# Optimization experiments

Measured on AMD Instinct MI355X. Metric: run time of the kernel, lower is better.

## Reference

```python
import jax, jax.numpy as jnp
import numpy as np

LOG2 = float(np.log(2.0))

def ssp(x):
    # shifted softplus used by SchNet
    return jax.nn.softplus(x) - LOG2

def setup_inputs() -> dict:
    N, E, DIM, RBF = 100000, 1600000, 64, 64
    key = jax.random.key(0)
    ks = jax.random.split(key, 20)
    def w(k, fan_in, fan_out):
        # xavier_uniform
        lim = float(np.sqrt(6.0 / (fan_in + fan_out)))
        return jax.random.uniform(k, (fan_in, fan_out), jnp.float32, -lim, lim)
    inp = {
        "node_feats": jax.random.normal(ks[0], (N, DIM), jnp.float32),
        "edge_feats": jax.random.normal(ks[1], (E, RBF), jnp.float32),
        "src": jax.random.randint(ks[2], (E,), 0, N, jnp.int32),
        "dst": jax.random.randint(ks[3], (E,), 0, N, jnp.int32),
        # EdgeUpdate.project_edge: Linear(2*dim+rbf, 2*dim) -> ssp -> Linear(2*dim, rbf)
        "eu_w1": w(ks[4], 2 * DIM + RBF, 2 * DIM), "eu_b1": jnp.zeros((2 * DIM,), jnp.float32),
        "eu_w2": w(ks[5], 2 * DIM, RBF), "eu_b2": jnp.zeros((RBF,), jnp.float32),
        # EUCFConv.project_node1: Linear(dim, dim) -> ssp (output unused by the original forward)
        "pn1_w": w(ks[6], DIM, DIM), "pn1_b": jnp.zeros((DIM,), jnp.float32),
        # EUCFConv.project_edge: Linear(rbf, dim) -> ssp -> Linear(dim, dim)
        "pe_w1": w(ks[7], RBF, DIM), "pe_b1": jnp.zeros((DIM,), jnp.float32),
        "pe_w2": w(ks[8], DIM, DIM), "pe_b2": jnp.zeros((DIM,), jnp.float32),
        # EUCFConv.project_node2: Linear(dim, dim) -> ssp -> Linear(dim, dim)
        "pn2_w1": w(ks[9], DIM, DIM), "pn2_b1": jnp.zeros((DIM,), jnp.float32),
        "pn2_w2": w(ks[10], DIM, DIM), "pn2_b2": jnp.zeros((DIM,), jnp.float32),
    }
    return inp

def reference(node_feats, edge_feats, src, dst,
              eu_w1, eu_b1, eu_w2, eu_b2,
              pn1_w, pn1_b,
              pe_w1, pe_b1, pe_w2, pe_b2,
              pn2_w1, pn2_b1, pn2_w2, pn2_b2):
    N = node_feats.shape[0]
    # ---- EdgeUpdate: gather src/dst node feats, concat with rbf, 2-layer MLP ----
    edge_h = jnp.concatenate(
        [node_feats[src], node_feats[dst], edge_feats], axis=-1)  # [E, 2*dim+rbf]
    new_edge = ssp(edge_h @ eu_w1 + eu_b1) @ eu_w2 + eu_b2        # [E, rbf]
    # ---- EUCFConv ----
    # project_node1 is computed in the original but its output ('hv') is never used.
    he = ssp(new_edge @ pe_w1 + pe_b1) @ pe_w2 + pe_b2            # [E, dim]
    # copy_edge message + sum reduce at destination nodes
    agg = jax.ops.segment_sum(he, dst, num_segments=N)            # [N, dim]
    new_node = ssp(agg @ pn2_w1 + pn2_b1) @ pn2_w2 + pn2_b2      # [N, dim]
    return node_feats + new_node, new_edge
```

## Files before the change

kernel.cpp:

```cpp
#include <hip/hip_runtime.h>
#include <cstdint>
#include <cstddef>

#define DIM 64
#define RBF 64
#define NNODE 100000
#define NEDGE 1600000

#define ETHREADS 768
#define EWAVES 12
#define EBLOCKS 256
#define NBLOCKS 512

#define BUFW 136
#define BUFSZ (16 * BUFW)

#define E_LDS_BYTES 135424
#define N_LDS_BYTES 69120

typedef __attribute__((ext_vector_type(8))) short short8;
typedef __attribute__((ext_vector_type(4))) float f32x4;

__device__ __forceinline__ short f2bf(float f) {
    union { float f; uint32_t u; } v; v.f = f;
    uint32_t r = v.u + 0x7fffu + ((v.u >> 16) & 1u);
    return (short)(r >> 16);
}

__device__ __forceinline__ float sspf(float x) {
    float h = __builtin_amdgcn_logf(1.0f + __builtin_amdgcn_exp2f(x * 1.44269504f));
    return 0.69314718f * (h - 1.0f);
}

__device__ void stage_bfrags(const float* __restrict__ W, short* dst,
                             int KB, int NT, int NCOLS, int tid, int nthr) {
    int total = KB * NT * 64;
    for (int s = tid; s < total; s += nthr) {
        int lane = s & 63;
        int g = s >> 6;
        int nt = g % NT;
        int kb = g / NT;
        int k0 = kb * 32 + ((lane >> 4) << 3);
        int col = nt * 16 + (lane & 15);
        short8 v;
        #pragma unroll
        for (int j = 0; j < 8; j++) v[j] = f2bf(W[(k0 + j) * NCOLS + col]);
        ((short8*)dst)[s] = v;
    }
}

__global__ __launch_bounds__(ETHREADS) void edge_kernel(
    const float* __restrict__ nf, const float* __restrict__ ef,
    const int* __restrict__ src, const int* __restrict__ dst,
    const float* __restrict__ eu_w1, const float* __restrict__ eu_b1,
    const float* __restrict__ eu_w2, const float* __restrict__ eu_b2,
    const float* __restrict__ pe_w1, const float* __restrict__ pe_b1,
    const float* __restrict__ pe_w2, const float* __restrict__ pe_b2,
    float* __restrict__ agg, float* __restrict__ out_edge)
{
    extern __shared__ char smem[];
    short* wB   = (short*)smem;
    float* bias = (float*)(smem + 81920);
    short* bufs = (short*)(smem + 83200);

    int tid = threadIdx.x;
    stage_bfrags(eu_w1, wB,         6, 8, 128, tid, ETHREADS);
    stage_bfrags(eu_w2, wB + 24576, 4, 4, 64,  tid, ETHREADS);
    stage_bfrags(pe_w1, wB + 32768, 2, 4, 64,  tid, ETHREADS);
    stage_bfrags(pe_w2, wB + 36864, 2, 4, 64,  tid, ETHREADS);
    for (int i = tid; i < 128; i += ETHREADS) bias[i] = eu_b1[i];
    for (int i = tid; i < 64; i += ETHREADS) {
        bias[128 + i] = eu_b2[i];
        bias[192 + i] = pe_b1[i];
        bias[256 + i] = pe_b2[i];
    }
    __syncthreads();

    const int wave = tid >> 6;
    const int lane = tid & 63;
    const int q = lane >> 4;
    const int c = lane & 15;
    short* buf = bufs + wave * BUFSZ;

    const short8* B1 = (const short8*)wB;
    const short8* B2 = (const short8*)(wB + 24576);
    const short8* B3 = (const short8*)(wB + 32768);
    const short8* B4 = (const short8*)(wB + 36864);

    const int numTiles = NEDGE / 16;
    for (int t = blockIdx.x * EWAVES + wave; t < numTiles; t += gridDim.x * EWAVES) {
        const int e0 = t * 16;
        const int es = src[e0 + c];
        const int ed = dst[e0 + c];
        const float* psrc = nf + (size_t)es * DIM;
        const float* pdst = nf + (size_t)ed * DIM;
        const float* pe   = ef + (size_t)(e0 + c) * RBF;

        f32x4 acc1[8];
        #pragma unroll
        for (int i = 0; i < 8; i++) acc1[i] = (f32x4){0.f, 0.f, 0.f, 0.f};
        #pragma unroll
        for (int kb = 0; kb < 6; kb++) {
            const float* bp = (kb < 2) ? psrc : (kb < 4) ? pdst : pe;
            int off = (kb & 1) * 32 + q * 8;
            float4 p0 = *(const float4*)(bp + off);
            float4 p1 = *(const float4*)(bp + off + 4);
            short8 a;
            a[0] = f2bf(p0.x); a[1] = f2bf(p0.y); a[2] = f2bf(p0.z); a[3] = f2bf(p0.w);
            a[4] = f2bf(p1.x); a[5] = f2bf(p1.y); a[6] = f2bf(p1.z); a[7] = f2bf(p1.w);
            #pragma unroll
            for (int nt = 0; nt < 8; nt++)
                acc1[nt] = __builtin_amdgcn_mfma_f32_16x16x32_bf16(
                    a, B1[(kb * 8 + nt) * 64 + lane], acc1[nt], 0, 0, 0);
        }
        #pragma unroll
        for (int nt = 0; nt < 8; nt++)
            #pragma unroll
            for (int r = 0; r < 4; r++)
                buf[(q * 4 + r) * BUFW + nt * 16 + c] =
                    f2bf(sspf(acc1[nt][r] + bias[nt * 16 + c]));

        short8 a2[4];
        #pragma unroll
        for (int kb = 0; kb < 4; kb++)
            a2[kb] = *(const short8*)(buf + c * BUFW + kb * 32 + q * 8);
        f32x4 acc2[4];
        #pragma unroll
        for (int i = 0; i < 4; i++) acc2[i] = (f32x4){0.f, 0.f, 0.f, 0.f};
        #pragma unroll
        for (int kb = 0; kb < 4; kb++)
            #pragma unroll
            for (int nt = 0; nt < 4; nt++)
                acc2[nt] = __builtin_amdgcn_mfma_f32_16x16x32_bf16(
                    a2[kb], B2[(kb * 4 + nt) * 64 + lane], acc2[nt], 0, 0, 0);
        #pragma unroll
        for (int nt = 0; nt < 4; nt++)
            #pragma unroll
            for (int r = 0; r < 4; r++) {
                float v = acc2[nt][r] + bias[128 + nt * 16 + c];
                out_edge[(size_t)(e0 + q * 4 + r) * RBF + nt * 16 + c] = v;
                buf[(q * 4 + r) * BUFW + nt * 16 + c] = f2bf(v);
            }

        short8 a3[2];
        #pragma unroll
        for (int kb = 0; kb < 2; kb++)
            a3[kb] = *(const short8*)(buf + c * BUFW + kb * 32 + q * 8);
        f32x4 acc3[4];
        #pragma unroll
        for (int i = 0; i < 4; i++) acc3[i] = (f32x4){0.f, 0.f, 0.f, 0.f};
        #pragma unroll
        for (int kb = 0; kb < 2; kb++)
            #pragma unroll
            for (int nt = 0; nt < 4; nt++)
                acc3[nt] = __builtin_amdgcn_mfma_f32_16x16x32_bf16(
                    a3[kb], B3[(kb * 4 + nt) * 64 + lane], acc3[nt], 0, 0, 0);
        #pragma unroll
        for (int nt = 0; nt < 4; nt++)
            #pragma unroll
            for (int r = 0; r < 4; r++)
                buf[(q * 4 + r) * BUFW + nt * 16 + c] =
                    f2bf(sspf(acc3[nt][r] + bias[192 + nt * 16 + c]));

        short8 a4[2];
        #pragma unroll
        for (int kb = 0; kb < 2; kb++)
            a4[kb] = *(const short8*)(buf + c * BUFW + kb * 32 + q * 8);
        f32x4 acc4[4];
        #pragma unroll
        for (int i = 0; i < 4; i++) acc4[i] = (f32x4){0.f, 0.f, 0.f, 0.f};
        #pragma unroll
        for (int kb = 0; kb < 2; kb++)
            #pragma unroll
            for (int nt = 0; nt < 4; nt++)
                acc4[nt] = __builtin_amdgcn_mfma_f32_16x16x32_bf16(
                    a4[kb], B4[(kb * 4 + nt) * 64 + lane], acc4[nt], 0, 0, 0);
        int drow[4];
        #pragma unroll
        for (int r = 0; r < 4; r++) drow[r] = dst[e0 + q * 4 + r];
        #pragma unroll
        for (int nt = 0; nt < 4; nt++)
            #pragma unroll
            for (int r = 0; r < 4; r++) {
                float v = acc4[nt][r] + bias[256 + nt * 16 + c];
                atomicAdd(&agg[(size_t)drow[r] * DIM + nt * 16 + c], v);
            }
    }
}

__global__ __launch_bounds__(ETHREADS) void node_kernel(
    const float* __restrict__ nf,
    const float* __restrict__ pn2_w1, const float* __restrict__ pn2_b1,
    const float* __restrict__ pn2_w2, const float* __restrict__ pn2_b2,
    float* __restrict__ out_node )
{
    extern __shared__ char smem[];
    short* wB   = (short*)smem;
    float* bias = (float*)(smem + 16384);
    short* bufs = (short*)(smem + 16896);

    int tid = threadIdx.x;
    stage_bfrags(pn2_w1, wB,        2, 4, 64, tid, ETHREADS);
    stage_bfrags(pn2_w2, wB + 4096, 2, 4, 64, tid, ETHREADS);
    for (int i = tid; i < 64; i += ETHREADS) {
        bias[i]      = pn2_b1[i];
        bias[64 + i] = pn2_b2[i];
    }
    __syncthreads();

    const int wave = tid >> 6;
    const int lane = tid & 63;
    const int q = lane >> 4;
    const int c = lane & 15;
    short* buf = bufs + wave * BUFSZ;
    const short8* B1 = (const short8*)wB;
    const short8* B2 = (const short8*)(wB + 4096);

    const int numTiles = NNODE / 16;
    for (int t = blockIdx.x * EWAVES + wave; t < numTiles; t += gridDim.x * EWAVES) {
        const int n0 = t * 16;
        const float* prow = out_node + (size_t)(n0 + c) * DIM;

        f32x4 acc1[4];
        #pragma unroll
        for (int i = 0; i < 4; i++) acc1[i] = (f32x4){0.f, 0.f, 0.f, 0.f};
        #pragma unroll
        for (int kb = 0; kb < 2; kb++) {
            int off = kb * 32 + q * 8;
            float4 p0 = *(const float4*)(prow + off);
            float4 p1 = *(const float4*)(prow + off + 4);
            short8 a;
            a[0] = f2bf(p0.x); a[1] = f2bf(p0.y); a[2] = f2bf(p0.z); a[3] = f2bf(p0.w);
            a[4] = f2bf(p1.x); a[5] = f2bf(p1.y); a[6] = f2bf(p1.z); a[7] = f2bf(p1.w);
            #pragma unroll
            for (int nt = 0; nt < 4; nt++)
                acc1[nt] = __builtin_amdgcn_mfma_f32_16x16x32_bf16(
                    a, B1[(kb * 4 + nt) * 64 + lane], acc1[nt], 0, 0, 0);
        }
        #pragma unroll
        for (int nt = 0; nt < 4; nt++)
            #pragma unroll
            for (int r = 0; r < 4; r++)
                buf[(q * 4 + r) * BUFW + nt * 16 + c] =
                    f2bf(sspf(acc1[nt][r] + bias[nt * 16 + c]));

        short8 a2[2];
        #pragma unroll
        for (int kb = 0; kb < 2; kb++)
            a2[kb] = *(const short8*)(buf + c * BUFW + kb * 32 + q * 8);
        f32x4 acc2[4];
        #pragma unroll
        for (int i = 0; i < 4; i++) acc2[i] = (f32x4){0.f, 0.f, 0.f, 0.f};
        #pragma unroll
        for (int kb = 0; kb < 2; kb++)
            #pragma unroll
            for (int nt = 0; nt < 4; nt++)
                acc2[nt] = __builtin_amdgcn_mfma_f32_16x16x32_bf16(
                    a2[kb], B2[(kb * 4 + nt) * 64 + lane], acc2[nt], 0, 0, 0);

        #pragma unroll
        for (int nt = 0; nt < 4; nt++)
            #pragma unroll
            for (int r = 0; r < 4; r++) {
                size_t idx = (size_t)(n0 + q * 4 + r) * DIM + nt * 16 + c;
                out_node[idx] = nf[idx] + acc2[nt][r] + bias[64 + nt * 16 + c];
            }
    }
}

extern "C" void kernel_launch(void* const* d_in, const int* in_sizes, int n_in,
                              void* d_out, int out_size, void* d_ws, size_t ws_size,
                              hipStream_t stream) {
    const float* nf     = (const float*)d_in[0];
    const float* ef     = (const float*)d_in[1];
    const int*   src    = (const int*)d_in[2];
    const int*   dst    = (const int*)d_in[3];
    const float* eu_w1  = (const float*)d_in[4];
    const float* eu_b1  = (const float*)d_in[5];
    const float* eu_w2  = (const float*)d_in[6];
    const float* eu_b2  = (const float*)d_in[7];
    const float* pe_w1  = (const float*)d_in[10];
    const float* pe_b1  = (const float*)d_in[11];
    const float* pe_w2  = (const float*)d_in[12];
    const float* pe_b2  = (const float*)d_in[13];
    const float* pn2_w1 = (const float*)d_in[14];
    const float* pn2_b1 = (const float*)d_in[15];
    const float* pn2_w2 = (const float*)d_in[16];
    const float* pn2_b2 = (const float*)d_in[17];

    float* out_node = (float*)d_out;
    float* out_edge = out_node + (size_t)NNODE * DIM;

    (void)d_ws; (void)ws_size; (void)in_sizes; (void)n_in; (void)out_size;

    (void)hipFuncSetAttribute((const void*)edge_kernel,
                              hipFuncAttributeMaxDynamicSharedMemorySize, E_LDS_BYTES);
    (void)hipFuncSetAttribute((const void*)node_kernel,
                              hipFuncAttributeMaxDynamicSharedMemorySize, N_LDS_BYTES);

    (void)hipMemsetAsync(out_node, 0, (size_t)NNODE * DIM * sizeof(float), stream);

    edge_kernel<<<EBLOCKS, ETHREADS, E_LDS_BYTES, stream>>>(
        nf, ef, src, dst, eu_w1, eu_b1, eu_w2, eu_b2,
        pe_w1, pe_b1, pe_w2, pe_b2, out_node, out_edge);

    node_kernel<<<NBLOCKS, ETHREADS, N_LDS_BYTES, stream>>>(
        nf, pn2_w1, pn2_b1, pn2_w2, pn2_b2, out_node);
}
```

Baseline: 1.016 ms.

## Software-pipeline edge gathers, use packed bf16 converts, and widen edge blocks

The edge kernel now prefetches the next tile's src/dst indices and gathered node/edge rows into registers while the current tile's MLP runs, so gather latency overlaps with MFMA work. Scalar bf16 rounding is replaced with the packed v_cvt_pk_bf16_f32 instruction. The per-tile dst reload for the scatter is replaced with wave shuffles. Edge blocks grow from 12 to 16 waves with an occupancy hint in launch_bounds. The 12 extra prefetch registers (float4 raw[12]) and the larger block raise register and LDS pressure, which could cause spills or lower occupancy.

After: 961.2 us. -5.4%, faster.

```diff
diff --git a/kernel.cpp b/kernel.cpp
--- a/kernel.cpp
+++ b/kernel.cpp
@@ -7,16 +7,19 @@
 #define NNODE 100000
 #define NEDGE 1600000
 
-#define ETHREADS 768
-#define EWAVES 12
+#define ETHREADS 1024
+#define EWAVES 16
 #define EBLOCKS 256
+
+#define NTHREADS 768
+#define NWAVES 12
 #define NBLOCKS 512
 
 #define BUFW 136
 #define BUFSZ (16 * BUFW)
 
-#define E_LDS_BYTES 135424
-#define N_LDS_BYTES 69120
+#define E_LDS_BYTES (83200 + EWAVES * BUFSZ * 2)
+#define N_LDS_BYTES (16896 + NWAVES * BUFSZ * 2)
 
 typedef __attribute__((ext_vector_type(8))) short short8;
 typedef __attribute__((ext_vector_type(4))) float f32x4;
@@ -25,6 +28,27 @@
     union { float f; uint32_t u; } v; v.f = f;
     uint32_t r = v.u + 0x7fffu + ((v.u >> 16) & 1u);
     return (short)(r >> 16);
+}
+
+__device__ __forceinline__ uint32_t cvtpk2(float lo, float hi) {
+    uint32_t r;
+    asm("v_cvt_pk_bf16_f32 %0, %1, %2" : "=v"(r) : "v"(lo), "v"(hi));
+    return r;
+}
+
+__device__ __forceinline__ short8 mk_afrag(float4 p0, float4 p1) {
+    union { short8 s; uint32_t u[4]; } r;
+    r.u[0] = cvtpk2(p0.x, p0.y);
+    r.u[1] = cvtpk2(p0.z, p0.w);
+    r.u[2] = cvtpk2(p1.x, p1.y);
+    r.u[3] = cvtpk2(p1.z, p1.w);
+    return r.s;
+}
+
+__device__ __forceinline__ void store_bf2(short* a, short* b, float x, float y) {
+    uint32_t w = cvtpk2(x, y);
+    *a = (short)w;
+    *b = (short)(w >> 16);
 }
 
 __device__ __forceinline__ float sspf(float x) {
@@ -49,7 +73,7 @@
     }
 }
 
-__global__ __launch_bounds__(ETHREADS) void edge_kernel(
+__global__ __launch_bounds__(ETHREADS, 4) void edge_kernel(
     const float* __restrict__ nf, const float* __restrict__ ef,
     const int* __restrict__ src, const int* __restrict__ dst,
     const float* __restrict__ eu_w1, const float* __restrict__ eu_b1,
@@ -88,37 +112,70 @@
     const short8* B4 = (const short8*)(wB + 36864);
 
     const int numTiles = NEDGE / 16;
-    for (int t = blockIdx.x * EWAVES + wave; t < numTiles; t += gridDim.x * EWAVES) {
+    const int stride = gridDim.x * EWAVES;
+    const int o0 = q * 8, o1 = 32 + q * 8;
+
+    int t = blockIdx.x * EWAVES + wave;
+
+    int cs_cur = src[t * 16 + c];
+    int cd_cur = dst[t * 16 + c];
+    float4 raw[12];
+    {
+        const float* ps = nf + (size_t)cs_cur * DIM;
+        const float* pd = nf + (size_t)cd_cur * DIM;
+        const float* pe = ef + (size_t)(t * 16 + c) * RBF;
+        raw[0]  = *(const float4*)(ps + o0); raw[1]  = *(const float4*)(ps + o0 + 4);
+        raw[2]  = *(const float4*)(ps + o1); raw[3]  = *(const float4*)(ps + o1 + 4);
+        raw[4]  = *(const float4*)(pd + o0); raw[5]  = *(const float4*)(pd + o0 + 4);
+        raw[6]  = *(const float4*)(pd + o1); raw[7]  = *(const float4*)(pd + o1 + 4);
+        raw[8]  = *(const float4*)(pe + o0); raw[9]  = *(const float4*)(pe + o0 + 4);
+        raw[10] = *(const float4*)(pe + o1); raw[11] = *(const float4*)(pe + o1 + 4);
+    }
+    int tn = t + stride;
+    int ns = 0, nd = 0;
+    if (tn < numTiles) { ns = src[tn * 16 + c]; nd = dst[tn * 16 + c]; }
+
+    while (true) {
         const int e0 = t * 16;
-        const int es = src[e0 + c];
-        const int ed = dst[e0 + c];
-        const float* psrc = nf + (size_t)es * DIM;
-        const float* pdst = nf + (size_t)ed * DIM;
-        const float* pe   = ef + (size_t)(e0 + c) * RBF;
+        const int edst = cd_cur;
 
         f32x4 acc1[8];
         #pragma unroll
         for (int i = 0; i < 8; i++) acc1[i] = (f32x4){0.f, 0.f, 0.f, 0.f};
         #pragma unroll
         for (int kb = 0; kb < 6; kb++) {
-            const float* bp = (kb < 2) ? psrc : (kb < 4) ? pdst : pe;
-            int off = (kb & 1) * 32 + q * 8;
-            float4 p0 = *(const float4*)(bp + off);
-            float4 p1 = *(const float4*)(bp + off + 4);
-            short8 a;
-            a[0] = f2bf(p0.x); a[1] = f2bf(p0.y); a[2] = f2bf(p0.z); a[3] = f2bf(p0.w);
-            a[4] = f2bf(p1.x); a[5] = f2bf(p1.y); a[6] = f2bf(p1.z); a[7] = f2bf(p1.w);
+            short8 a = mk_afrag(raw[2 * kb], raw[2 * kb + 1]);
             #pragma unroll
             for (int nt = 0; nt < 8; nt++)
                 acc1[nt] = __builtin_amdgcn_mfma_f32_16x16x32_bf16(
                     a, B1[(kb * 8 + nt) * 64 + lane], acc1[nt], 0, 0, 0);
         }
         #pragma unroll
-        for (int nt = 0; nt < 8; nt++)
-            #pragma unroll
-            for (int r = 0; r < 4; r++)
-                buf[(q * 4 + r) * BUFW + nt * 16 + c] =
-                    f2bf(sspf(acc1[nt][r] + bias[nt * 16 + c]));
+        for (int nt = 0; nt < 8; nt++) {
+            float b = bias[nt * 16 + c];
+            float v0 = sspf(acc1[nt][0] + b);
+            float v1 = sspf(acc1[nt][1] + b);
+            float v2 = sspf(acc1[nt][2] + b);
+            float v3 = sspf(acc1[nt][3] + b);
+            short* p = buf + nt * 16 + c;
+            store_bf2(p + (q * 4 + 0) * BUFW, p + (q * 4 + 1) * BUFW, v0, v1);
+            store_bf2(p + (q * 4 + 2) * BUFW, p + (q * 4 + 3) * BUFW, v2, v3);
+        }
+
+        if (tn < numTiles) {
+            const float* ps = nf + (size_t)ns * DIM;
+            const float* pd = nf + (size_t)nd * DIM;
+            const float* pe = ef + (size_t)(tn * 16 + c) * RBF;
+            raw[0]  = *(const float4*)(ps + o0); raw[1]  = *(const float4*)(ps + o0 + 4);
+            raw[2]  = *(const float4*)(ps + o1); raw[3]  = *(const float4*)(ps + o1 + 4);
+            raw[4]  = *(const float4*)(pd + o0); raw[5]  = *(const float4*)(pd + o0 + 4);
+            raw[6]  = *(const float4*)(pd + o1); raw[7]  = *(const float4*)(pd + o1 + 4);
+            raw[8]  = *(const float4*)(pe + o0); raw[9]  = *(const float4*)(pe + o0 + 4);
+            raw[10] = *(const float4*)(pe + o1); raw[11] = *(const float4*)(pe + o1 + 4);
+            cd_cur = nd;
+            int t2 = tn + stride;
+            if (t2 < numTiles) { ns = src[t2 * 16 + c]; nd = dst[t2 * 16 + c]; }
+        }
 
         short8 a2[4];
         #pragma unroll
@@ -134,13 +191,20 @@
                 acc2[nt] = __builtin_amdgcn_mfma_f32_16x16x32_bf16(
                     a2[kb], B2[(kb * 4 + nt) * 64 + lane], acc2[nt], 0, 0, 0);
         #pragma unroll
-        for (int nt = 0; nt < 4; nt++)
-            #pragma unroll
-            for (int r = 0; r < 4; r++) {
-                float v = acc2[nt][r] + bias[128 + nt * 16 + c];
-                out_edge[(size_t)(e0 + q * 4 + r) * RBF + nt * 16 + c] = v;
-                buf[(q * 4 + r) * BUFW + nt * 16 + c] = f2bf(v);
-            }
+        for (int nt = 0; nt < 4; nt++) {
+            float b = bias[128 + nt * 16 + c];
+            float w0 = acc2[nt][0] + b;
+            float w1 = acc2[nt][1] + b;
+            float w2 = acc2[nt][2] + b;
+            float w3 = acc2[nt][3] + b;
+            out_edge[(size_t)(e0 + q * 4 + 0) * RBF + nt * 16 + c] = w0;
+            out_edge[(size_t)(e0 + q * 4 + 1) * RBF + nt * 16 + c] = w1;
+            out_edge[(size_t)(e0 + q * 4 + 2) * RBF + nt * 16 + c] = w2;
+            out_edge[(size_t)(e0 + q * 4 + 3) * RBF + nt * 16 + c] = w3;
+            short* p = buf + nt * 16 + c;
+            store_bf2(p + (q * 4 + 0) * BUFW, p + (q * 4 + 1) * BUFW, w0, w1);
+            store_bf2(p + (q * 4 + 2) * BUFW, p + (q * 4 + 3) * BUFW, w2, w3);
+        }
 
         short8 a3[2];
         #pragma unroll
@@ -156,11 +220,16 @@
                 acc3[nt] = __builtin_amdgcn_mfma_f32_16x16x32_bf16(
                     a3[kb], B3[(kb * 4 + nt) * 64 + lane], acc3[nt], 0, 0, 0);
         #pragma unroll
-        for (int nt = 0; nt < 4; nt++)
-            #pragma unroll
-            for (int r = 0; r < 4; r++)
-                buf[(q * 4 + r) * BUFW + nt * 16 + c] =
-                    f2bf(sspf(acc3[nt][r] + bias[192 + nt * 16 + c]));
+        for (int nt = 0; nt < 4; nt++) {
+            float b = bias[192 + nt * 16 + c];
+            float v0 = sspf(acc3[nt][0] + b);
+            float v1 = sspf(acc3[nt][1] + b);
+            float v2 = sspf(acc3[nt][2] + b);
+            float v3 = sspf(acc3[nt][3] + b);
+            short* p = buf + nt * 16 + c;
+            store_bf2(p + (q * 4 + 0) * BUFW, p + (q * 4 + 1) * BUFW, v0, v1);
+            store_bf2(p + (q * 4 + 2) * BUFW, p + (q * 4 + 3) * BUFW, v2, v3);
+        }
 
         short8 a4[2];
         #pragma unroll
@@ -175,20 +244,25 @@
             for (int nt = 0; nt < 4; nt++)
                 acc4[nt] = __builtin_amdgcn_mfma_f32_16x16x32_bf16(
                     a4[kb], B4[(kb * 4 + nt) * 64 + lane], acc4[nt], 0, 0, 0);
-        int drow[4];
-        #pragma unroll
-        for (int r = 0; r < 4; r++) drow[r] = dst[e0 + q * 4 + r];
-        #pragma unroll
-        for (int nt = 0; nt < 4; nt++)
-            #pragma unroll
-            for (int r = 0; r < 4; r++) {
-                float v = acc4[nt][r] + bias[256 + nt * 16 + c];
-                atomicAdd(&agg[(size_t)drow[r] * DIM + nt * 16 + c], v);
-            }
-    }
-}
-
-__global__ __launch_bounds__(ETHREADS) void node_kernel(
+        int drow0 = __shfl(edst, q * 4 + 0, 64);
+        int drow1 = __shfl(edst, q * 4 + 1, 64);
+        int drow2 = __shfl(edst, q * 4 + 2, 64);
+        int drow3 = __shfl(edst, q * 4 + 3, 64);
+        #pragma unroll
+        for (int nt = 0; nt < 4; nt++) {
+            float b = bias[256 + nt * 16 + c];
+            atomicAdd(&agg[(size_t)drow0 * DIM + nt * 16 + c], acc4[nt][0] + b);
+            atomicAdd(&agg[(size_t)drow1 * DIM + nt * 16 + c], acc4[nt][1] + b);
+            atomicAdd(&agg[(size_t)drow2 * DIM + nt * 16 + c], acc4[nt][2] + b);
+            atomicAdd(&agg[(size_t)drow3 * DIM + nt * 16 + c], acc4[nt][3] + b);
+        }
+
+        if (tn >= numTiles) break;
+        t = tn; tn += stride;
+    }
+}
+
+__global__ __launch_bounds__(NTHREADS) void node_kernel(
     const float* __restrict__ nf,
     const float* __restrict__ pn2_w1, const float* __restrict__ pn2_b1,
     const float* __restrict__ pn2_w2, const float* __restrict__ pn2_b2,
@@ -200,9 +274,9 @@
     short* bufs = (short*)(smem + 16896);
 
     int tid = threadIdx.x;
-    stage_bfrags(pn2_w1, wB,        2, 4, 64, tid, ETHREADS);
-    stage_bfrags(pn2_w2, wB + 4096, 2, 4, 64, tid, ETHREADS);
-    for (int i = tid; i < 64; i += ETHREADS) {
+    stage_bfrags(pn2_w1, wB,        2, 4, 64, tid, NTHREADS);
+    stage_bfrags(pn2_w2, wB + 4096, 2, 4, 64, tid, NTHREADS);
+    for (int i = tid; i < 64; i += NTHREADS) {
         bias[i]      = pn2_b1[i];
         bias[64 + i] = pn2_b2[i];
     }
@@ -217,7 +291,7 @@
     const short8* B2 = (const short8*)(wB + 4096);
 
     const int numTiles = NNODE / 16;
-    for (int t = blockIdx.x * EWAVES + wave; t < numTiles; t += gridDim.x * EWAVES) {
+    for (int t = blockIdx.x * NWAVES + wave; t < numTiles; t += gridDim.x * NWAVES) {
         const int n0 = t * 16;
         const float* prow = out_node + (size_t)(n0 + c) * DIM;
 
@@ -229,20 +303,23 @@
             int off = kb * 32 + q * 8;
             float4 p0 = *(const float4*)(prow + off);
             float4 p1 = *(const float4*)(prow + off + 4);
-            short8 a;
-            a[0] = f2bf(p0.x); a[1] = f2bf(p0.y); a[2] = f2bf(p0.z); a[3] = f2bf(p0.w);
-            a[4] = f2bf(p1.x); a[5] = f2bf(p1.y); a[6] = f2bf(p1.z); a[7] = f2bf(p1.w);
+            short8 a = mk_afrag(p0, p1);
             #pragma unroll
             for (int nt = 0; nt < 4; nt++)
                 acc1[nt] = __builtin_amdgcn_mfma_f32_16x16x32_bf16(
                     a, B1[(kb * 4 + nt) * 64 + lane], acc1[nt], 0, 0, 0);
         }
         #pragma unroll
-        for (int nt = 0; nt < 4; nt++)
-            #pragma unroll
-            for (int r = 0; r < 4; r++)
-                buf[(q * 4 + r) * BUFW + nt * 16 + c] =
-                    f2bf(sspf(acc1[nt][r] + bias[nt * 16 + c]));
+        for (int nt = 0; nt < 4; nt++) {
+            float b = bias[nt * 16 + c];
+            float v0 = sspf(acc1[nt][0] + b);
+            float v1 = sspf(acc1[nt][1] + b);
+            float v2 = sspf(acc1[nt][2] + b);
+            float v3 = sspf(acc1[nt][3] + b);
+            short* p = buf + nt * 16 + c;
+            store_bf2(p + (q * 4 + 0) * BUFW, p + (q * 4 + 1) * BUFW, v0, v1);
+            store_bf2(p + (q * 4 + 2) * BUFW, p + (q * 4 + 3) * BUFW, v2, v3);
+        }
 
         short8 a2[2];
         #pragma unroll
@@ -304,6 +381,6 @@
         nf, ef, src, dst, eu_w1, eu_b1, eu_w2, eu_b2,
         pe_w1, pe_b1, pe_w2, pe_b2, out_node, out_edge);
 
-    node_kernel<<<NBLOCKS, ETHREADS, N_LDS_BYTES, stream>>>(
+    node_kernel<<<NBLOCKS, NTHREADS, N_LDS_BYTES, stream>>>(
         nf, pn2_w1, pn2_b1, pn2_w2, pn2_b2, out_node);
 }
```
